# Kernel optimization log

Measured on AMD Instinct MI355X. Metric: run time of the kernel, lower is better.

Reference implementation:

```python
import jax, jax.numpy as jnp
import numpy as np
from jax import lax

# dims: B=2, C=dim=64, H=W=128 -> N=16384 tokens; d_inner=128, d_state=16, dt_rank=4, d_conv=4

def setup_inputs() -> dict:
    key = jax.random.key(0)
    ks = jax.random.split(key, 8)
    def n(k, shp, scale=0.02):
        return jax.random.normal(k, shp, jnp.float32) * scale
    d_inner, d_state, dt_rank = 128, 16, 4
    return {
        "x": jax.random.normal(ks[0], (2, 64, 128, 128), jnp.float32),
        "ln_w": jnp.ones((64,), jnp.float32),
        "ln_b": jnp.zeros((64,), jnp.float32),
        "in_proj_w": n(ks[1], (2 * d_inner, 64)),
        "conv_w": n(ks[2], (d_inner, 1, 4), 0.1),
        "conv_b": jnp.zeros((d_inner,), jnp.float32),
        "x_proj_w": n(ks[3], (dt_rank + 2 * d_state, d_inner)),
        "dt_proj_w": n(ks[4], (d_inner, dt_rank), 0.5),
        "dt_proj_b": n(ks[5], (d_inner,), 0.1),
        "A_log": jnp.log(jnp.broadcast_to(jnp.arange(1, d_state + 1, dtype=jnp.float32), (d_inner, d_state))),
        "D_param": jnp.ones((d_inner,), jnp.float32),
        "out_proj_w": n(ks[6], (64, d_inner)),
        "out_proj_b": jnp.zeros((64,), jnp.float32),
    }


def reference(x, ln_w, ln_b, in_proj_w, conv_w, conv_b, x_proj_w,
              dt_proj_w, dt_proj_b, A_log, D_param, out_proj_w, out_proj_b):
    B, C, H, W = x.shape
    d_inner = in_proj_w.shape[0] // 2
    d_state = A_log.shape[1]
    dt_rank = dt_proj_w.shape[1]
    eps = 1e-5

    # feature2token + channel LayerNorm (Restormer WithBias LN over C)
    t = x.reshape(B, C, H * W).transpose(0, 2, 1)  # [B, N, C]
    mu = jnp.mean(t, axis=-1, keepdims=True)
    var = jnp.var(t, axis=-1, keepdims=True)
    t = (t - mu) * lax.rsqrt(var + eps) * ln_w + ln_b

    # in_proj -> x, z
    xz = jnp.einsum('bnc,dc->bnd', t, in_proj_w)  # [B, N, 2*d_inner]
    x_in, z = jnp.split(xz, 2, axis=-1)

    # depthwise causal conv1d (k=4, pad left 3), then SiLU
    u = lax.conv_general_dilated(
        x_in.transpose(0, 2, 1), conv_w,
        window_strides=(1,), padding=[(3, 0)],
        feature_group_count=d_inner,
        dimension_numbers=('NCH', 'OIH', 'NCH'))
    u = jax.nn.silu(u + conv_b[None, :, None]).transpose(0, 2, 1)  # [B, N, d_inner]

    # x_proj -> dt, B, C of the SSM
    x_dbl = jnp.einsum('bnd,ed->bne', u, x_proj_w)
    dt_r = x_dbl[..., :dt_rank]
    Bmat = x_dbl[..., dt_rank:dt_rank + d_state]   # [B, N, d_state]
    Cmat = x_dbl[..., dt_rank + d_state:]          # [B, N, d_state]
    dt = jax.nn.softplus(jnp.einsum('bnr,dr->bnd', dt_r, dt_proj_w) + dt_proj_b)

    # selective scan: h_t = exp(dt*A) h_{t-1} + dt*B*u
    A = -jnp.exp(A_log)  # [d_inner, d_state]
    deltaA = jnp.exp(jnp.einsum('bnd,ds->bnds', dt, A))
    deltaBu = jnp.einsum('bnd,bns,bnd->bnds', dt, Bmat, u)

    def combine(c1, c2):
        a1, b1 = c1
        a2, b2 = c2
        return a2 * a1, a2 * b1 + b2

    _, h = lax.associative_scan(combine, (deltaA, deltaBu), axis=1)  # h: [B, N, d_inner, d_state]

    y = jnp.einsum('bnds,bns->bnd', h, Cmat) + u * D_param
    y = y * jax.nn.silu(z)
    out = jnp.einsum('bnd,cd->bnc', y, out_proj_w) + out_proj_b  # [B, N, C]

    # token2feature
    return out.transpose(0, 2, 1).reshape(B, C, H, W)
```

## Files before the change

kernel.cpp:

```cpp
#include <hip/hip_runtime.h>
#include <math.h>

#define NTOK 16384
#define DIN  128
#define NCH  512
#define CHL  32
#define NG   32
#define GCH  16

__device__ __forceinline__ float silu_f(float x)    { return x / (1.f + __expf(-x)); }
__device__ __forceinline__ float softplus_f(float x){ return (x > 20.f) ? x : log1pf(__expf(x)); }

__global__ __launch_bounds__(256) void k1_ln_inproj(
    const float* __restrict__ x, const float* __restrict__ lnw,
    const float* __restrict__ lnb, const float* __restrict__ Win,
    float* __restrict__ xin, float* __restrict__ zbuf)
{
  __shared__ __align__(16) float bufW[128*68];
  __shared__ __align__(16) float bufB[64*68];
  __shared__ float ps[256], pq[256], mu[64], rs[64];

  int t = threadIdx.x;
  int b  = blockIdx.x >> 8;
  int n0 = (blockIdx.x & 255) << 6;
  const float* xb = x + ((size_t)b*64)*NTOK;

  int tok = t & 63, quad = t >> 6;
  float s0 = 0.f, s1 = 0.f;
  for (int i = 0; i < 16; ++i) {
    int c = i*4 + quad;
    float v = xb[(size_t)c*NTOK + n0 + tok];
    bufW[c*68 + tok] = v;
    s0 += v; s1 += v*v;
  }
  ps[t] = s0; pq[t] = s1;
  __syncthreads();
  if (t < 64) {
    float m = ps[t] + ps[64+t] + ps[128+t] + ps[192+t];
    float q = pq[t] + pq[64+t] + pq[128+t] + pq[192+t];
    m *= 0.015625f;
    q = q*0.015625f - m*m;
    mu[t] = m; rs[t] = rsqrtf(q + 1e-5f);
  }
  __syncthreads();

  {
    int c = t & 63, tq = t >> 6;
    float wv = lnw[c], bv = lnb[c];
    #pragma unroll
    for (int i = 0; i < 4; ++i) {
      int tok4 = tq*4 + i;
      float4 f = *(const float4*)&bufW[c*68 + tok4*4];
      float vals[4] = {f.x, f.y, f.z, f.w};
      #pragma unroll
      for (int k = 0; k < 4; ++k) {
        int tk = tok4*4 + k;
        bufB[tk*68 + c] = (vals[k] - mu[tk]) * rs[tk] * wv + bv;
      }
    }
  }

  int tokg = t & 7, dg = t >> 3;
  const float4* TB = (const float4*)bufB;
  const float4* TW = (const float4*)bufW;
  long nbase = (long)b*NTOK + n0;
  for (int half = 0; half < 2; ++half) {
    __syncthreads();
    {
      const float4* Wg = (const float4*)&Win[(half << 7)*64];
      #pragma unroll
      for (int i = 0; i < 8; ++i) {
        int idx = i*256 + t;
        int row = idx >> 4, q = idx & 15;
        *(float4*)&bufW[row*68 + q*4] = Wg[row*16 + q];
      }
    }
    __syncthreads();
    float acc[8][4];
    #pragma unroll
    for (int i = 0; i < 8; ++i)
      #pragma unroll
      for (int j = 0; j < 4; ++j) acc[i][j] = 0.f;
    #pragma unroll 4
    for (int c4 = 0; c4 < 16; ++c4) {
      float4 tv[8], wv[4];
      #pragma unroll
      for (int i = 0; i < 8; ++i) tv[i] = TB[(tokg + 8*i)*17 + c4];
      #pragma unroll
      for (int j = 0; j < 4; ++j) wv[j] = TW[(dg + 32*j)*17 + c4];
      #pragma unroll
      for (int i = 0; i < 8; ++i)
        #pragma unroll
        for (int j = 0; j < 4; ++j)
          acc[i][j] += tv[i].x*wv[j].x + tv[i].y*wv[j].y
                     + tv[i].z*wv[j].z + tv[i].w*wv[j].w;
    }
    #pragma unroll
    for (int i = 0; i < 8; ++i) {
      long n = nbase + tokg + 8*i;
      #pragma unroll
      for (int j = 0; j < 4; ++j) {
        int d = dg + 32*j;
        if (half == 0) xin[n*128 + d] = acc[i][j];
        else           zbuf[n*128 + d] = silu_f(acc[i][j]);
      }
    }
  }
}

__global__ __launch_bounds__(256) void k2_conv(
    const float* __restrict__ xin, const float* __restrict__ cw,
    const float* __restrict__ cb, float* __restrict__ u)
{
  int t = threadIdx.x;
  int d = t & 127;
  long g0 = (long)blockIdx.x*16 + (t >> 7)*8;
  int n = (int)(g0 & (NTOK-1));
  float w0 = cw[d*4], w1 = cw[d*4+1], w2 = cw[d*4+2], w3 = cw[d*4+3];
  float cbv = cb[d];
  float xa = (n >= 3) ? xin[(g0-3)*128 + d] : 0.f;
  float xb = (n >= 2) ? xin[(g0-2)*128 + d] : 0.f;
  float xc = (n >= 1) ? xin[(g0-1)*128 + d] : 0.f;
  #pragma unroll
  for (int j = 0; j < 8; ++j) {
    float xd = xin[(g0+j)*128 + d];
    u[(g0+j)*128 + d] = silu_f(w0*xa + w1*xb + w2*xc + w3*xd + cbv);
    xa = xb; xb = xc; xc = xd;
  }
}

__global__ __launch_bounds__(256) void k3_xproj_dt(
    const float* __restrict__ u, const float* __restrict__ Wx,
    const float* __restrict__ Wdt, const float* __restrict__ db,
    float* __restrict__ dt, float* __restrict__ Bm, float* __restrict__ Cm)
{
  __shared__ __align__(16) float wx[36*128];
  __shared__ float wdtT[4*128];
  __shared__ __align__(16) float xdbl[64*40];
  int t = threadIdx.x;
  for (int i = t; i < 1152; i += 256)
    *(float4*)&wx[i*4] = *(const float4*)&Wx[i*4];
  for (int i = t; i < 512; i += 256)
    wdtT[(i&3)*128 + (i>>2)] = Wdt[i];
  __syncthreads();

  long tok0 = (long)blockIdx.x * 64;
  int tok = t & 63, grp = t >> 6;
  const float* urow = u + (tok0 + tok)*128;

  float acc[9];
  #pragma unroll
  for (int e = 0; e < 9; ++e) acc[e] = 0.f;
  #pragma unroll 8
  for (int d4 = 0; d4 < 32; ++d4) {
    float4 uv = *(const float4*)&urow[d4*4];
    #pragma unroll
    for (int e = 0; e < 9; ++e) {
      float4 wv = *(const float4*)&wx[(grp*9+e)*128 + d4*4];
      acc[e] += uv.x*wv.x + uv.y*wv.y + uv.z*wv.z + uv.w*wv.w;
    }
  }
  #pragma unroll
  for (int e = 0; e < 9; ++e) xdbl[tok*40 + grp*9 + e] = acc[e];
  __syncthreads();

  {
    int tk = t >> 2, q = t & 3;
    float4 bv = *(const float4*)&xdbl[tk*40 + 4  + q*4];
    float4 cv = *(const float4*)&xdbl[tk*40 + 20 + q*4];
    *(float4*)&Bm[(tok0+tk)*16 + q*4] = bv;
    *(float4*)&Cm[(tok0+tk)*16 + q*4] = cv;
  }
  int d = t & 127, th = t >> 7;
  float w0 = wdtT[d], w1 = wdtT[128+d], w2 = wdtT[256+d], w3 = wdtT[384+d];
  float bias = db[d];
  for (int j = 0; j < 32; ++j) {
    int tk = th*32 + j;
    float a = bias + xdbl[tk*40]*w0 + xdbl[tk*40+1]*w1
                   + xdbl[tk*40+2]*w2 + xdbl[tk*40+3]*w3;
    dt[(tok0+tk)*128 + d] = softplus_f(a);
  }
}

__global__ __launch_bounds__(256) void k4a_local(
    const float* __restrict__ dt, const float* __restrict__ u,
    const float* __restrict__ Bm, const float* __restrict__ Alog,
    float* __restrict__ carP, float* __restrict__ carH)
{
  int t = threadIdx.x;
  int d = t >> 1, sh = t & 1;
  int b = blockIdx.x / NCH, ch = blockIdx.x % NCH;
  long nb = (long)b*NTOK + (long)ch*CHL;
  float A[8], h[8], P[8];
  #pragma unroll
  for (int k = 0; k < 2; ++k) {
    float4 a = *(const float4*)&Alog[d*16 + sh*8 + k*4];
    A[k*4+0] = -__expf(a.x); A[k*4+1] = -__expf(a.y);
    A[k*4+2] = -__expf(a.z); A[k*4+3] = -__expf(a.w);
  }
  #pragma unroll
  for (int s = 0; s < 8; ++s) { h[s] = 0.f; P[s] = 1.f; }
  for (int i = 0; i < CHL; ++i) {
    long n = nb + i;
    float dtv = dt[n*128 + d];
    float uv  = u [n*128 + d];
    float du  = dtv * uv;
    float Bv[8];
    #pragma unroll
    for (int k = 0; k < 2; ++k) {
      float4 v = *(const float4*)&Bm[n*16 + sh*8 + k*4];
      Bv[k*4]=v.x; Bv[k*4+1]=v.y; Bv[k*4+2]=v.z; Bv[k*4+3]=v.w;
    }
    #pragma unroll
    for (int s = 0; s < 8; ++s) {
      float dA = __expf(dtv * A[s]);
      h[s] = dA*h[s] + du*Bv[s];
      P[s] *= dA;
    }
  }
  long cbs = ((long)(b*NCH + ch)*128 + d)*16 + sh*8;
  #pragma unroll
  for (int k = 0; k < 2; ++k) {
    *(float4*)&carP[cbs + k*4] = make_float4(P[k*4],P[k*4+1],P[k*4+2],P[k*4+3]);
    *(float4*)&carH[cbs + k*4] = make_float4(h[k*4],h[k*4+1],h[k*4+2],h[k*4+3]);
  }
}

__global__ __launch_bounds__(256) void k4b1_group(
    float* __restrict__ cP, float* __restrict__ cH,
    float* __restrict__ Pg, float* __restrict__ Hg)
{
  int idx = blockIdx.x*256 + threadIdx.x;
  int rem = idx & 2047;
  int g   = (idx >> 11) & (NG-1);
  int b   = idx >> 16;
  float P = 1.f, H = 0.f;
  long base = ((long)b*NCH + g*GCH)*2048 + rem;
  #pragma unroll 4
  for (int j = 0; j < GCH; ++j) {
    long a = base + (long)j*2048;
    float p = cP[a], h = cH[a];
    cP[a] = P; cH[a] = H;
    H = p*H + h;
    P = p*P;
  }
  long ga = ((long)b*NG + g)*2048 + rem;
  Pg[ga] = P; Hg[ga] = H;
}

__global__ __launch_bounds__(256) void k4b2_carry(
    const float* __restrict__ Pg, float* __restrict__ Hg)
{
  int idx = blockIdx.x*256 + threadIdx.x;
  int b = idx >> 11, rem = idx & 2047;
  float H = 0.f;
  #pragma unroll 4
  for (int g = 0; g < NG; ++g) {
    long a = ((long)b*NG + g)*2048 + rem;
    float p = Pg[a], h = Hg[a];
    Hg[a] = H;
    H = p*H + h;
  }
}

__global__ __launch_bounds__(256) void k4c_apply(
    const float* __restrict__ dt, const float* __restrict__ u,
    const float* __restrict__ Bm, const float* __restrict__ Cm,
    const float* __restrict__ Alog, const float* __restrict__ Dp,
    const float* __restrict__ zs, const float* __restrict__ pPre,
    const float* __restrict__ hPre, const float* __restrict__ Hg,
    float* __restrict__ yz)
{
  int t = threadIdx.x;
  int d = t >> 1, sh = t & 1;
  int b = blockIdx.x / NCH, ch = blockIdx.x % NCH;
  long nb = (long)b*NTOK + (long)ch*CHL;
  float A[8], h[8];
  #pragma unroll
  for (int k = 0; k < 2; ++k) {
    float4 a = *(const float4*)&Alog[d*16 + sh*8 + k*4];
    A[k*4+0] = -__expf(a.x); A[k*4+1] = -__expf(a.y);
    A[k*4+2] = -__expf(a.z); A[k*4+3] = -__expf(a.w);
  }
  long cbs = ((long)(b*NCH + ch)*128 + d)*16 + sh*8;
  long gbs = ((long)b*NG + (ch >> 4))*2048 + d*16 + sh*8;
  #pragma unroll
  for (int k = 0; k < 2; ++k) {
    float4 hp = *(const float4*)&hPre[cbs + k*4];
    float4 pp = *(const float4*)&pPre[cbs + k*4];
    float4 gi = *(const float4*)&Hg[gbs + k*4];
    h[k*4+0] = hp.x + pp.x*gi.x; h[k*4+1] = hp.y + pp.y*gi.y;
    h[k*4+2] = hp.z + pp.z*gi.z; h[k*4+3] = hp.w + pp.w*gi.w;
  }
  float Dv = Dp[d];
  for (int i = 0; i < CHL; ++i) {
    long n = nb + i;
    float dtv = dt[n*128 + d];
    float uv  = u [n*128 + d];
    float du  = dtv * uv;
    float Bv[8], Cv[8];
    #pragma unroll
    for (int k = 0; k < 2; ++k) {
      float4 v = *(const float4*)&Bm[n*16 + sh*8 + k*4];
      Bv[k*4]=v.x; Bv[k*4+1]=v.y; Bv[k*4+2]=v.z; Bv[k*4+3]=v.w;
      float4 w = *(const float4*)&Cm[n*16 + sh*8 + k*4];
      Cv[k*4]=w.x; Cv[k*4+1]=w.y; Cv[k*4+2]=w.z; Cv[k*4+3]=w.w;
    }
    float y = 0.f;
    #pragma unroll
    for (int s = 0; s < 8; ++s) {
      float dA = __expf(dtv * A[s]);
      h[s] = dA*h[s] + du*Bv[s];
      y += h[s]*Cv[s];
    }
    y += __shfl_xor(y, 1);
    if (sh == 0)
      yz[n*128 + d] = (y + uv*Dv) * zs[n*128 + d];
  }
}

__global__ __launch_bounds__(256) void k6_outproj(
    const float* __restrict__ yz, const float* __restrict__ Wout,
    const float* __restrict__ ob, float* __restrict__ out)
{
  __shared__ __align__(16) float wo[64*132];
  __shared__ __align__(16) float yl[32*132];
  int t = threadIdx.x;
  long tok0 = (long)blockIdx.x * 32;
  for (int i = 0; i < 8; ++i) {
    int g = i*256 + t; int c = g >> 5, q = g & 31;
    *(float4*)&wo[c*132 + q*4] = *(const float4*)&Wout[c*128 + q*4];
  }
  for (int i = 0; i < 4; ++i) {
    int g = i*256 + t; int tok = g >> 5, q = g & 31;
    *(float4*)&yl[tok*132 + q*4] = *(const float4*)&yz[(tok0 + tok)*128 + q*4];
  }
  __syncthreads();
  int tp = t & 15;
  int tg = t >> 4;
  float acc[4][2] = {{0.f}};
  for (int d4 = 0; d4 < 32; ++d4) {
    float4 y0 = *(const float4*)&yl[tg*132 + d4*4];
    float4 y1 = *(const float4*)&yl[(tg+16)*132 + d4*4];
    #pragma unroll
    for (int cc = 0; cc < 4; ++cc) {
      float4 wv = *(const float4*)&wo[(tp + 16*cc)*132 + d4*4];
      acc[cc][0] += wv.x*y0.x + wv.y*y0.y + wv.z*y0.z + wv.w*y0.w;
      acc[cc][1] += wv.x*y1.x + wv.y*y1.y + wv.z*y1.z + wv.w*y1.w;
    }
  }
  int b  = (int)(tok0 / NTOK);
  long n0 = tok0 % NTOK;
  #pragma unroll
  for (int cc = 0; cc < 4; ++cc) {
    int c = tp + 16*cc;
    float bias = ob[c];
    out[((long)b*64 + c)*NTOK + n0 + tg     ] = acc[cc][0] + bias;
    out[((long)b*64 + c)*NTOK + n0 + tg + 16] = acc[cc][1] + bias;
  }
}

extern "C" void kernel_launch(void* const* d_in, const int* in_sizes, int n_in,
                              void* d_out, int out_size, void* d_ws, size_t ws_size,
                              hipStream_t stream)
{
  (void)in_sizes; (void)n_in; (void)out_size; (void)ws_size;
  const float* x    = (const float*)d_in[0];
  const float* lnw  = (const float*)d_in[1];
  const float* lnb  = (const float*)d_in[2];
  const float* Win  = (const float*)d_in[3];
  const float* cw   = (const float*)d_in[4];
  const float* cb   = (const float*)d_in[5];
  const float* Wx   = (const float*)d_in[6];
  const float* Wdt  = (const float*)d_in[7];
  const float* db   = (const float*)d_in[8];
  const float* Alog = (const float*)d_in[9];
  const float* Dp   = (const float*)d_in[10];
  const float* Wout = (const float*)d_in[11];
  const float* ob   = (const float*)d_in[12];
  float* out = (float*)d_out;

  float* w   = (float*)d_ws;
  float* xin = w;
  float* z   = w + 4194304;
  float* u   = w + 8388608;
  float* dt  = w + 12582912;
  float* Bm  = w + 16777216;
  float* Cm  = w + 17301504;
  float* cP  = w + 17825792;
  float* cH  = w + 19922944;
  float* Pg  = w + 22020096;
  float* Hg  = w + 22151168;
  float* yz  = w + 22282240;

  k1_ln_inproj<<<512, 256, 0, stream>>>(x, lnw, lnb, Win, xin, z);
  k2_conv     <<<2048,256, 0, stream>>>(xin, cw, cb, u);
  k3_xproj_dt <<<512, 256, 0, stream>>>(u, Wx, Wdt, db, dt, Bm, Cm);
  k4a_local   <<<1024,256, 0, stream>>>(dt, u, Bm, Alog, cP, cH);
  k4b1_group  <<<512, 256, 0, stream>>>(cP, cH, Pg, Hg);
  k4b2_carry  <<<16,  256, 0, stream>>>(Pg, Hg);
  k4c_apply   <<<1024,256, 0, stream>>>(dt, u, Bm, Cm, Alog, Dp, z, cP, cH, Hg, yz);
  k6_outproj  <<<1024,256, 0, stream>>>(yz, Wout, ob, out);
}
```

Measured before the change: 148.8 us.

## Fuse x_proj/dt with local chunk scan and retile in_proj GEMM

The dt/x_proj kernel and the per-chunk local scan kernel are merged into one. Each block computes dt and B in shared memory and immediately runs the 32-token chunk scan over all 16 states per channel, which avoids re-reading dt, u and B from global memory and removes a kernel launch. The trade-off is higher register pressure (16-state arrays) and half as many threads doing the serial scan. Separately, the LN+in_proj kernel is retiled to compute xin and z in one accumulator pass over C halves, with an 8x8 register tile per thread.

```diff
diff --git a/kernel.cpp b/kernel.cpp
--- a/kernel.cpp
+++ b/kernel.cpp
@@ -16,7 +16,7 @@
     const float* __restrict__ lnb, const float* __restrict__ Win,
     float* __restrict__ xin, float* __restrict__ zbuf)
 {
-  __shared__ __align__(16) float bufW[128*68];
+  __shared__ __align__(16) float bufW[256*36];
   __shared__ __align__(16) float bufB[64*68];
   __shared__ float ps[256], pq[256], mu[64], rs[64];
 
@@ -60,51 +60,50 @@
     }
   }
 
-  int tokg = t & 7, dg = t >> 3;
+  int tokg = t >> 5, dg = t & 31;
   const float4* TB = (const float4*)bufB;
   const float4* TW = (const float4*)bufW;
-  long nbase = (long)b*NTOK + n0;
+  float acc[8][8];
+  #pragma unroll
+  for (int i = 0; i < 8; ++i)
+    #pragma unroll
+    for (int j = 0; j < 8; ++j) acc[i][j] = 0.f;
+
   for (int half = 0; half < 2; ++half) {
     __syncthreads();
-    {
-      const float4* Wg = (const float4*)&Win[(half << 7)*64];
-      #pragma unroll
-      for (int i = 0; i < 8; ++i) {
-        int idx = i*256 + t;
-        int row = idx >> 4, q = idx & 15;
-        *(float4*)&bufW[row*68 + q*4] = Wg[row*16 + q];
-      }
+    #pragma unroll
+    for (int i = 0; i < 8; ++i) {
+      int idx = i*256 + t;
+      int row = idx >> 3, q = idx & 7;
+      *(float4*)&bufW[row*36 + q*4] = *(const float4*)&Win[row*64 + half*32 + q*4];
     }
     __syncthreads();
-    float acc[8][4];
-    #pragma unroll
-    for (int i = 0; i < 8; ++i)
-      #pragma unroll
-      for (int j = 0; j < 4; ++j) acc[i][j] = 0.f;
-    #pragma unroll 4
-    for (int c4 = 0; c4 < 16; ++c4) {
-      float4 tv[8], wv[4];
-      #pragma unroll
-      for (int i = 0; i < 8; ++i) tv[i] = TB[(tokg + 8*i)*17 + c4];
-      #pragma unroll
-      for (int j = 0; j < 4; ++j) wv[j] = TW[(dg + 32*j)*17 + c4];
+    #pragma unroll
+    for (int c4 = 0; c4 < 8; ++c4) {
+      float4 tv[8], wv[8];
+      #pragma unroll
+      for (int i = 0; i < 8; ++i) tv[i] = TB[(tokg + 8*i)*17 + half*8 + c4];
+      #pragma unroll
+      for (int j = 0; j < 8; ++j) wv[j] = TW[(dg + 32*j)*9 + c4];
       #pragma unroll
       for (int i = 0; i < 8; ++i)
         #pragma unroll
-        for (int j = 0; j < 4; ++j)
+        for (int j = 0; j < 8; ++j)
           acc[i][j] += tv[i].x*wv[j].x + tv[i].y*wv[j].y
                      + tv[i].z*wv[j].z + tv[i].w*wv[j].w;
     }
-    #pragma unroll
-    for (int i = 0; i < 8; ++i) {
-      long n = nbase + tokg + 8*i;
-      #pragma unroll
-      for (int j = 0; j < 4; ++j) {
-        int d = dg + 32*j;
-        if (half == 0) xin[n*128 + d] = acc[i][j];
-        else           zbuf[n*128 + d] = silu_f(acc[i][j]);
-      }
-    }
+  }
+
+  long nbase = (long)b*NTOK + n0;
+  #pragma unroll
+  for (int i = 0; i < 8; ++i) {
+    long n = nbase + tokg + 8*i;
+    #pragma unroll
+    for (int j = 0; j < 4; ++j)
+      xin[n*128 + dg + 32*j] = acc[i][j];
+    #pragma unroll
+    for (int j = 4; j < 8; ++j)
+      zbuf[n*128 + dg + 32*(j-4)] = silu_f(acc[i][j]);
   }
 }
 
@@ -129,10 +128,12 @@
   }
 }
 
-__global__ __launch_bounds__(256) void k3_xproj_dt(
+__global__ __launch_bounds__(256) void k34(
     const float* __restrict__ u, const float* __restrict__ Wx,
     const float* __restrict__ Wdt, const float* __restrict__ db,
-    float* __restrict__ dt, float* __restrict__ Bm, float* __restrict__ Cm)
+    const float* __restrict__ Alog,
+    float* __restrict__ dt, float* __restrict__ Bm, float* __restrict__ Cm,
+    float* __restrict__ carP, float* __restrict__ carH)
 {
   __shared__ __align__(16) float wx[36*128];
   __shared__ float wdtT[4*128];
@@ -145,23 +146,24 @@
   __syncthreads();
 
   long tok0 = (long)blockIdx.x * 64;
-  int tok = t & 63, grp = t >> 6;
-  const float* urow = u + (tok0 + tok)*128;
-
-  float acc[9];
-  #pragma unroll
-  for (int e = 0; e < 9; ++e) acc[e] = 0.f;
-  #pragma unroll 8
-  for (int d4 = 0; d4 < 32; ++d4) {
-    float4 uv = *(const float4*)&urow[d4*4];
-    #pragma unroll
-    for (int e = 0; e < 9; ++e) {
-      float4 wv = *(const float4*)&wx[(grp*9+e)*128 + d4*4];
-      acc[e] += uv.x*wv.x + uv.y*wv.y + uv.z*wv.z + uv.w*wv.w;
-    }
-  }
-  #pragma unroll
-  for (int e = 0; e < 9; ++e) xdbl[tok*40 + grp*9 + e] = acc[e];
+  {
+    int tok = t & 63, grp = t >> 6;
+    const float* urow = u + (tok0 + tok)*128;
+    float acc[9];
+    #pragma unroll
+    for (int e = 0; e < 9; ++e) acc[e] = 0.f;
+    #pragma unroll 8
+    for (int d4 = 0; d4 < 32; ++d4) {
+      float4 uv = *(const float4*)&urow[d4*4];
+      #pragma unroll
+      for (int e = 0; e < 9; ++e) {
+        float4 wv = *(const float4*)&wx[(grp*9+e)*128 + d4*4];
+        acc[e] += uv.x*wv.x + uv.y*wv.y + uv.z*wv.z + uv.w*wv.w;
+      }
+    }
+    #pragma unroll
+    for (int e = 0; e < 9; ++e) xdbl[tok*40 + grp*9 + e] = acc[e];
+  }
   __syncthreads();
 
   {
@@ -171,56 +173,45 @@
     *(float4*)&Bm[(tok0+tk)*16 + q*4] = bv;
     *(float4*)&Cm[(tok0+tk)*16 + q*4] = cv;
   }
+
   int d = t & 127, th = t >> 7;
   float w0 = wdtT[d], w1 = wdtT[128+d], w2 = wdtT[256+d], w3 = wdtT[384+d];
   float bias = db[d];
-  for (int j = 0; j < 32; ++j) {
-    int tk = th*32 + j;
-    float a = bias + xdbl[tk*40]*w0 + xdbl[tk*40+1]*w1
-                   + xdbl[tk*40+2]*w2 + xdbl[tk*40+3]*w3;
-    dt[(tok0+tk)*128 + d] = softplus_f(a);
-  }
-}
-
-__global__ __launch_bounds__(256) void k4a_local(
-    const float* __restrict__ dt, const float* __restrict__ u,
-    const float* __restrict__ Bm, const float* __restrict__ Alog,
-    float* __restrict__ carP, float* __restrict__ carH)
-{
-  int t = threadIdx.x;
-  int d = t >> 1, sh = t & 1;
-  int b = blockIdx.x / NCH, ch = blockIdx.x % NCH;
-  long nb = (long)b*NTOK + (long)ch*CHL;
-  float A[8], h[8], P[8];
-  #pragma unroll
-  for (int k = 0; k < 2; ++k) {
-    float4 a = *(const float4*)&Alog[d*16 + sh*8 + k*4];
+  float A[16], h[16], P[16];
+  #pragma unroll
+  for (int k = 0; k < 4; ++k) {
+    float4 a = *(const float4*)&Alog[d*16 + k*4];
     A[k*4+0] = -__expf(a.x); A[k*4+1] = -__expf(a.y);
     A[k*4+2] = -__expf(a.z); A[k*4+3] = -__expf(a.w);
   }
   #pragma unroll
-  for (int s = 0; s < 8; ++s) { h[s] = 0.f; P[s] = 1.f; }
-  for (int i = 0; i < CHL; ++i) {
-    long n = nb + i;
-    float dtv = dt[n*128 + d];
-    float uv  = u [n*128 + d];
-    float du  = dtv * uv;
-    float Bv[8];
-    #pragma unroll
-    for (int k = 0; k < 2; ++k) {
-      float4 v = *(const float4*)&Bm[n*16 + sh*8 + k*4];
+  for (int s = 0; s < 16; ++s) { h[s] = 0.f; P[s] = 1.f; }
+  long g0 = tok0 + th*32;
+  for (int j = 0; j < CHL; ++j) {
+    int tk = th*32 + j;
+    float4 xr = *(const float4*)&xdbl[tk*40];
+    float dtv = softplus_f(bias + xr.x*w0 + xr.y*w1 + xr.z*w2 + xr.w*w3);
+    long n = g0 + j;
+    dt[n*128 + d] = dtv;
+    float du = dtv * u[n*128 + d];
+    float Bv[16];
+    #pragma unroll
+    for (int k = 0; k < 4; ++k) {
+      float4 v = *(const float4*)&xdbl[tk*40 + 4 + k*4];
       Bv[k*4]=v.x; Bv[k*4+1]=v.y; Bv[k*4+2]=v.z; Bv[k*4+3]=v.w;
     }
     #pragma unroll
-    for (int s = 0; s < 8; ++s) {
+    for (int s = 0; s < 16; ++s) {
       float dA = __expf(dtv * A[s]);
       h[s] = dA*h[s] + du*Bv[s];
       P[s] *= dA;
     }
   }
-  long cbs = ((long)(b*NCH + ch)*128 + d)*16 + sh*8;
-  #pragma unroll
-  for (int k = 0; k < 2; ++k) {
+  int b = blockIdx.x >> 8;
+  int ch = (blockIdx.x & 255)*2 + th;
+  long cbs = ((long)(b*NCH + ch)*128 + d)*16;
+  #pragma unroll
+  for (int k = 0; k < 4; ++k) {
     *(float4*)&carP[cbs + k*4] = make_float4(P[k*4],P[k*4+1],P[k*4+2],P[k*4+3]);
     *(float4*)&carH[cbs + k*4] = make_float4(h[k*4],h[k*4+1],h[k*4+2],h[k*4+3]);
   }
@@ -395,8 +386,7 @@
 
   k1_ln_inproj<<<512, 256, 0, stream>>>(x, lnw, lnb, Win, xin, z);
   k2_conv     <<<2048,256, 0, stream>>>(xin, cw, cb, u);
-  k3_xproj_dt <<<512, 256, 0, stream>>>(u, Wx, Wdt, db, dt, Bm, Cm);
-  k4a_local   <<<1024,256, 0, stream>>>(dt, u, Bm, Alog, cP, cH);
+  k34         <<<512, 256, 0, stream>>>(u, Wx, Wdt, db, Alog, dt, Bm, Cm, cP, cH);
   k4b1_group  <<<512, 256, 0, stream>>>(cP, cH, Pg, Hg);
   k4b2_carry  <<<16,  256, 0, stream>>>(Pg, Hg);
   k4c_apply   <<<1024,256, 0, stream>>>(dt, u, Bm, Cm, Alog, Dp, z, cP, cH, Hg, yz);
```

Measured after the change: 213.3 us. 1.43x slower.

## Fuse x_proj/dt projection into local chunk scan kernel

Applied to the files above, without the earlier changes.

Merges the x_proj/dt kernel with the per-chunk local scan kernel. Each block loads its 32-token chunk of u into XOR-swizzled shared memory, computes the x_proj outputs there, and then runs the local scan directly from shared memory. This avoids re-reading dt, u and B from global memory and removes one launch. dt, B and C are still written out for the later apply kernel, and each block now reloads the x_proj weights for only 32 tokens instead of 64, which adds redundant weight traffic.

```diff
diff --git a/kernel.cpp b/kernel.cpp
--- a/kernel.cpp
+++ b/kernel.cpp
@@ -129,68 +129,68 @@
   }
 }
 
-__global__ __launch_bounds__(256) void k3_xproj_dt(
+__global__ __launch_bounds__(256) void k34(
     const float* __restrict__ u, const float* __restrict__ Wx,
     const float* __restrict__ Wdt, const float* __restrict__ db,
-    float* __restrict__ dt, float* __restrict__ Bm, float* __restrict__ Cm)
-{
-  __shared__ __align__(16) float wx[36*128];
-  __shared__ float wdtT[4*128];
-  __shared__ __align__(16) float xdbl[64*40];
+    const float* __restrict__ Alog,
+    float* __restrict__ dt, float* __restrict__ Bm, float* __restrict__ Cm,
+    float* __restrict__ carP, float* __restrict__ carH)
+{
+  __shared__ __align__(16) float sm[36*128 + 32*128];
+  float* wx   = sm;
+  float* ul   = sm + 4608;
+  float* xdbl = sm;
+
   int t = threadIdx.x;
+  int b  = blockIdx.x >> 9;
+  int ch = blockIdx.x & 511;
+  long tok0 = (long)b*NTOK + (long)ch*CHL;
+
   for (int i = t; i < 1152; i += 256)
     *(float4*)&wx[i*4] = *(const float4*)&Wx[i*4];
-  for (int i = t; i < 512; i += 256)
-    wdtT[(i&3)*128 + (i>>2)] = Wdt[i];
-  __syncthreads();
-
-  long tok0 = (long)blockIdx.x * 64;
-  int tok = t & 63, grp = t >> 6;
-  const float* urow = u + (tok0 + tok)*128;
-
-  float acc[9];
-  #pragma unroll
-  for (int e = 0; e < 9; ++e) acc[e] = 0.f;
+  #pragma unroll
+  for (int i = 0; i < 4; ++i) {
+    int idx = i*256 + t;
+    int tok = idx >> 5, d4 = idx & 31;
+    float4 v = *(const float4*)&u[(tok0 + tok)*128 + d4*4];
+    *(float4*)&ul[tok*128 + ((d4 ^ tok) << 2)] = v;
+  }
+  __syncthreads();
+
+  int tokx = t & 31, grp = t >> 5;
+  int base = (grp < 4) ? grp*5 : 20 + (grp-4)*4;
+  int ne   = (grp < 4) ? 5 : 4;
+  float acc[5];
+  #pragma unroll
+  for (int k = 0; k < 5; ++k) acc[k] = 0.f;
   #pragma unroll 8
   for (int d4 = 0; d4 < 32; ++d4) {
-    float4 uv = *(const float4*)&urow[d4*4];
-    #pragma unroll
-    for (int e = 0; e < 9; ++e) {
-      float4 wv = *(const float4*)&wx[(grp*9+e)*128 + d4*4];
-      acc[e] += uv.x*wv.x + uv.y*wv.y + uv.z*wv.z + uv.w*wv.w;
-    }
-  }
-  #pragma unroll
-  for (int e = 0; e < 9; ++e) xdbl[tok*40 + grp*9 + e] = acc[e];
+    float4 uv = *(const float4*)&ul[tokx*128 + ((d4 ^ tokx) << 2)];
+    #pragma unroll
+    for (int k = 0; k < 5; ++k) {
+      if (k < ne) {
+        float4 wv = *(const float4*)&wx[(base+k)*128 + d4*4];
+        acc[k] += uv.x*wv.x + uv.y*wv.y + uv.z*wv.z + uv.w*wv.w;
+      }
+    }
+  }
+  __syncthreads();
+  #pragma unroll
+  for (int k = 0; k < 5; ++k)
+    if (k < ne) xdbl[tokx*40 + base + k] = acc[k];
   __syncthreads();
 
   {
-    int tk = t >> 2, q = t & 3;
-    float4 bv = *(const float4*)&xdbl[tk*40 + 4  + q*4];
-    float4 cv = *(const float4*)&xdbl[tk*40 + 20 + q*4];
-    *(float4*)&Bm[(tok0+tk)*16 + q*4] = bv;
-    *(float4*)&Cm[(tok0+tk)*16 + q*4] = cv;
-  }
-  int d = t & 127, th = t >> 7;
-  float w0 = wdtT[d], w1 = wdtT[128+d], w2 = wdtT[256+d], w3 = wdtT[384+d];
+    int tk = (t & 127) >> 2, q = t & 3;
+    if (t < 128)
+      *(float4*)&Bm[(tok0+tk)*16 + q*4] = *(const float4*)&xdbl[tk*40 + 4  + q*4];
+    else
+      *(float4*)&Cm[(tok0+tk)*16 + q*4] = *(const float4*)&xdbl[tk*40 + 20 + q*4];
+  }
+
+  int d = t & 127, sh = t >> 7;
+  float4 wd = *(const float4*)&Wdt[d*4];
   float bias = db[d];
-  for (int j = 0; j < 32; ++j) {
-    int tk = th*32 + j;
-    float a = bias + xdbl[tk*40]*w0 + xdbl[tk*40+1]*w1
-                   + xdbl[tk*40+2]*w2 + xdbl[tk*40+3]*w3;
-    dt[(tok0+tk)*128 + d] = softplus_f(a);
-  }
-}
-
-__global__ __launch_bounds__(256) void k4a_local(
-    const float* __restrict__ dt, const float* __restrict__ u,
-    const float* __restrict__ Bm, const float* __restrict__ Alog,
-    float* __restrict__ carP, float* __restrict__ carH)
-{
-  int t = threadIdx.x;
-  int d = t >> 1, sh = t & 1;
-  int b = blockIdx.x / NCH, ch = blockIdx.x % NCH;
-  long nb = (long)b*NTOK + (long)ch*CHL;
   float A[8], h[8], P[8];
   #pragma unroll
   for (int k = 0; k < 2; ++k) {
@@ -200,15 +200,18 @@
   }
   #pragma unroll
   for (int s = 0; s < 8; ++s) { h[s] = 0.f; P[s] = 1.f; }
-  for (int i = 0; i < CHL; ++i) {
-    long n = nb + i;
-    float dtv = dt[n*128 + d];
-    float uv  = u [n*128 + d];
-    float du  = dtv * uv;
+  int dw = ((d >> 2)), dl = d & 3;
+  for (int j = 0; j < CHL; ++j) {
+    float4 xr = *(const float4*)&xdbl[j*40];
+    float dtv = softplus_f(bias + xr.x*wd.x + xr.y*wd.y + xr.z*wd.z + xr.w*wd.w);
+    long n = tok0 + j;
+    if (sh == 0) dt[n*128 + d] = dtv;
+    float uvv = ul[j*128 + ((dw ^ j) << 2) + dl];
+    float du = dtv * uvv;
     float Bv[8];
     #pragma unroll
     for (int k = 0; k < 2; ++k) {
-      float4 v = *(const float4*)&Bm[n*16 + sh*8 + k*4];
+      float4 v = *(const float4*)&xdbl[j*40 + 4 + sh*8 + k*4];
       Bv[k*4]=v.x; Bv[k*4+1]=v.y; Bv[k*4+2]=v.z; Bv[k*4+3]=v.w;
     }
     #pragma unroll
@@ -395,8 +398,7 @@
 
   k1_ln_inproj<<<512, 256, 0, stream>>>(x, lnw, lnb, Win, xin, z);
   k2_conv     <<<2048,256, 0, stream>>>(xin, cw, cb, u);
-  k3_xproj_dt <<<512, 256, 0, stream>>>(u, Wx, Wdt, db, dt, Bm, Cm);
-  k4a_local   <<<1024,256, 0, stream>>>(dt, u, Bm, Alog, cP, cH);
+  k34         <<<1024,256, 0, stream>>>(u, Wx, Wdt, db, Alog, dt, Bm, Cm, cP, cH);
   k4b1_group  <<<512, 256, 0, stream>>>(cP, cH, Pg, Hg);
   k4b2_carry  <<<16,  256, 0, stream>>>(Pg, Hg);
   k4c_apply   <<<1024,256, 0, stream>>>(dt, u, Bm, Cm, Alog, Dp, z, cP, cH, Hg, yz);
```

After: 156.1 us. +4.9%, slower.
